# Kernel optimization log

Measured on AMD Instinct MI355X. Metric: run time of the kernel, lower is better.

Reference implementation:

```python
import jax, jax.numpy as jnp
import numpy as np

B, N, DIM, H, DH, P = 4, 4096, 256, 8, 64, 2
INNER = H * DH  # 512


def setup_inputs() -> dict:
    key = jax.random.key(0)
    ks = jax.random.split(key, 10)
    w = lambda k, shape: jax.random.normal(k, shape, dtype=jnp.float32) * 0.02
    return dict(
        x=jax.random.normal(ks[0], (B, N, DIM), dtype=jnp.float32),
        prev_x=jax.random.normal(ks[1], (B, N, DIM), dtype=jnp.float32),
        ln_q_g=jnp.ones((2 * DIM,), jnp.float32), ln_q_b=jnp.zeros((2 * DIM,), jnp.float32),
        ln_k_g=jnp.ones((DIM,), jnp.float32), ln_k_b=jnp.zeros((DIM,), jnp.float32),
        ln_v_g=jnp.ones((DIM,), jnp.float32), ln_v_b=jnp.zeros((DIM,), jnp.float32),
        Wq=w(ks[2], (2 * DIM, INNER)),            # to_q, bias=False
        Wk=w(ks[3], (DIM, INNER)), bk=jnp.zeros((INNER,), jnp.float32),
        Wv=w(ks[4], (DIM, INNER)), bv=jnp.zeros((INNER,), jnp.float32),
        Woff=w(ks[5], (H * P, INNER)),            # 1x1 conv == linear over channels
        boff=jax.random.uniform(ks[6], (H * P,), jnp.float32, -1.0, 1.0),
        Wout=w(ks[7], (DIM, INNER)), bout=jnp.zeros((DIM,), jnp.float32),
    )


def _ln(x, g, b):
    m = x.mean(-1, keepdims=True)
    v = ((x - m) ** 2).mean(-1, keepdims=True)
    return (x - m) * jax.lax.rsqrt(v + 1e-5) * g + b


def reference(x, prev_x, ln_q_g, ln_q_b, ln_k_g, ln_k_b, ln_v_g, ln_v_b,
              Wq, Wk, bk, Wv, bv, Woff, boff, Wout, bout):
    scale = DH ** -0.5
    # queries from cat(x, prev_x) along feature dim
    q = _ln(jnp.concatenate([x, prev_x], axis=-1), ln_q_g, ln_q_b) @ Wq  # (B,N,INNER)
    # learned per-head, per-point offsets (1x1 conv over channels)
    offsets = (q @ Woff.T + boff).reshape(B, N, H, P).transpose(0, 2, 3, 1)  # (B,H,P,N)
    # K/V from cat(x, prev_x) along batch dim -> KV length 2N per (b,h)
    kv = jnp.concatenate([x, prev_x], axis=0)  # (2B,N,DIM)
    k = (_ln(kv, ln_k_g, ln_k_b) @ Wk + bk).reshape(2, B, N, H, DH).transpose(1, 3, 4, 0, 2).reshape(B, H, DH, 2 * N)
    v = (_ln(kv, ln_v_g, ln_v_b) @ Wv + bv).reshape(2, B, N, H, DH).transpose(1, 3, 4, 0, 2).reshape(B, H, DH, 2 * N)
    # sampling positions: pos + offset, clamped, truncated to int (matches torch .long())
    pos = jnp.arange(N, dtype=jnp.float32)
    samp = jnp.clip(pos[None, None, None, :] + offsets, 0, 2 * N - 1).astype(jnp.int32)  # (B,H,P,N)
    idx = samp.transpose(0, 1, 3, 2)[:, :, None, :, :]  # (B,H,1,N,P)
    k_s = jnp.take_along_axis(k[:, :, :, None, :], idx, axis=-1)  # (B,H,DH,N,P)
    v_s = jnp.take_along_axis(v[:, :, :, None, :], idx, axis=-1)  # (B,H,DH,N,P)
    qh = q.reshape(B, N, H, DH).transpose(0, 2, 1, 3) * scale     # (B,H,N,DH)
    sim = jnp.einsum('bhnd,bhdnp->bhnp', qh, k_s)                  # (B,H,N,P)
    attn = jax.nn.softmax(sim, axis=-1)
    out = jnp.einsum('bhnp,bhdnp->bhnd', attn, v_s)                # (B,H,N,DH)
    out = out.transpose(0, 2, 1, 3).reshape(B, N, INNER) @ Wout.T + bout  # (B,N,DIM)
    return out, offsets
```

## Files before the change

### kernel.cpp

```cpp
#include <hip/hip_runtime.h>
#include <hip/hip_bf16.h>
#include <math.h>

#define B_    4
#define N_    4096
#define DIM_  256
#define H_    8
#define DH_   64
#define P_    2
#define INNER_ 512
#define BN_   (B_ * N_)
#define KVR_  (2 * BN_)
#define VOFF_ ((size_t)H_ * KVR_ * DH_)

typedef short v8s  __attribute__((ext_vector_type(8)));
typedef short v4s  __attribute__((ext_vector_type(4)));
typedef float v4f  __attribute__((ext_vector_type(4)));

__device__ __forceinline__ short f2b(float x) {
    __hip_bfloat16 h = __float2bfloat16(x);
    return *reinterpret_cast<short*>(&h);
}
__device__ __forceinline__ float b2f(short s) {
    __hip_bfloat16 h = *reinterpret_cast<__hip_bfloat16*>(&s);
    return __bfloat162float(h);
}

__device__ __forceinline__ void async16(const void* g, void* l) {
    __builtin_amdgcn_global_load_lds(
        (const __attribute__((address_space(1))) void*)g,
        (__attribute__((address_space(3))) void*)l, 16, 0, 0);
}

__device__ __forceinline__ void storeRow(float* p, float4 f0, float4 f1, float4 f2, float4 f3) {
    ((float4*)p)[0] = f0; ((float4*)p)[1] = f1; ((float4*)p)[2] = f2; ((float4*)p)[3] = f3;
}
__device__ __forceinline__ void storeRowS(short* p, float4 f0, float4 f1, float4 f2, float4 f3) {
    v8s o0, o1;
    o0[0]=f2b(f0.x); o0[1]=f2b(f0.y); o0[2]=f2b(f0.z); o0[3]=f2b(f0.w);
    o0[4]=f2b(f1.x); o0[5]=f2b(f1.y); o0[6]=f2b(f1.z); o0[7]=f2b(f1.w);
    o1[0]=f2b(f2.x); o1[1]=f2b(f2.y); o1[2]=f2b(f2.z); o1[3]=f2b(f2.w);
    o1[4]=f2b(f3.x); o1[5]=f2b(f3.y); o1[6]=f2b(f3.z); o1[7]=f2b(f3.w);
    ((v8s*)p)[0] = o0; ((v8s*)p)[1] = o1;
}

__global__ __launch_bounds__(256) void prep_all(
    const float* __restrict__ Wq, const float* __restrict__ gq, const float* __restrict__ betaq,
    const float* __restrict__ Wk, const float* __restrict__ gk, const float* __restrict__ betak,
    const float* __restrict__ bk,
    const float* __restrict__ Wv, const float* __restrict__ gv, const float* __restrict__ betav,
    const float* __restrict__ bv,
    const float* __restrict__ Woff, const float* __restrict__ Wout,
    short* __restrict__ Wq2t, float* __restrict__ bq2,
    short* __restrict__ Wkvt, float* __restrict__ bkv,
    float* __restrict__ Wcomb, float* __restrict__ braw, short* __restrict__ Woutb) {
    __shared__ float sm[272];
    const int bid = blockIdx.x, t = threadIdx.x;

    if (bid < 1536) {
        const float *W, *g, *beta, *bias_in;
        short* Wt; float* b2; int K, n; float scale;
        if (bid < 512)       { W=Wq; g=gq; beta=betaq; bias_in=nullptr; Wt=Wq2t; b2=bq2; K=512; n=bid;        scale=0.125f; }
        else if (bid < 1024) { W=Wk; g=gk; beta=betak; bias_in=bk; Wt=Wkvt;           b2=bkv;       K=256; n=bid-512;  scale=1.f; }
        else                 { W=Wv; g=gv; beta=betav; bias_in=bv; Wt=Wkvt+512*256;   b2=bkv+512;   K=256; n=bid-1024; scale=1.f; }
        float partial = 0.f;
        for (int k = t; k < K; k += 256) {
            float w = W[k * 512 + n];
            Wt[(size_t)n * K + k] = f2b(scale * g[k] * w);
            partial += beta[k] * w;
        }
        sm[t] = partial;
        __syncthreads();
        for (int s = 128; s > 0; s >>= 1) {
            if (t < s) sm[t] += sm[t + s];
            __syncthreads();
        }
        if (t == 0) b2[n] = scale * ((bias_in ? bias_in[n] : 0.f) + sm[0]);
    } else if (bid < 2048) {
        const int k = bid - 1536;
        const int hp = t & 15, jg = t >> 4;
        float p = 0.f;
        for (int j = jg; j < INNER_; j += 16)
            p += Wq[k * INNER_ + j] * Woff[hp * INNER_ + j];
        sm[jg * 17 + hp] = p;
        __syncthreads();
        if (t < 16) {
            float s = 0.f;
            for (int i = 0; i < 16; i++) s += sm[i * 17 + t];
            Wcomb[k * 16 + t] = gq[k] * s;
            braw[k * 16 + t]  = betaq[k] * s;
        }
    } else {
        const int i0 = (bid - 2048) * 1024 + t * 4;
        float4 f = *(const float4*)(Wout + i0);
        v4s o;
        o[0] = f2b(f.x); o[1] = f2b(f.y); o[2] = f2b(f.z); o[3] = f2b(f.w);
        *(v4s*)(Woutb + i0) = o;
    }
}

__global__ __launch_bounds__(256) void norm_fused_kernel(
    const float* __restrict__ x, const float* __restrict__ p,
    const float* __restrict__ Wcomb, const float* __restrict__ braw,
    const float* __restrict__ boff,
    short* __restrict__ Aq, short* __restrict__ Akv,
    float* __restrict__ out_off, int* __restrict__ idx) {
    __shared__ float smr[272];
    __shared__ float sc[4][4][16][33];
    const int t    = threadIdx.x;
    const int lane = t & 63;
    const int wv   = t >> 6;
    const int m0   = (blockIdx.x * 4 + wv) * 4;
    const int k8   = lane * 8;

    {
        const int hp = t & 15, kg = t >> 4;
        float pp = 0.f;
        for (int k = kg; k < 512; k += 16) pp += braw[k * 16 + hp];
        smr[kg * 17 + hp] = pp;
    }
    __syncthreads();
    if (t < 16) {
        float s = 0.f;
#pragma unroll
        for (int i = 0; i < 16; i++) s += smr[i * 17 + t];
        smr[256 + t] = s + boff[t];
    }
    __syncthreads();

    float4 w[8][4];
#pragma unroll
    for (int i = 0; i < 8; i++) {
        const float4* wr = (const float4*)(Wcomb + (size_t)(k8 + i) * 16);
#pragma unroll
        for (int j = 0; j < 4; j++) w[i][j] = wr[j];
    }

    const float* srcb = (lane < 32) ? (x + k8) : (p + k8 - DIM_);

    float4 ua[4][2];
#pragma unroll
    for (int r = 0; r < 4; r++) {
        ua[r][0] = ((const float4*)(srcb + (size_t)(m0 + r) * DIM_))[0];
        ua[r][1] = ((const float4*)(srcb + (size_t)(m0 + r) * DIM_))[1];
    }

    float s[4], q2[4];
#pragma unroll
    for (int r = 0; r < 4; r++) {
        float uv[8] = { ua[r][0].x, ua[r][0].y, ua[r][0].z, ua[r][0].w,
                        ua[r][1].x, ua[r][1].y, ua[r][1].z, ua[r][1].w };
        float ss = 0.f, qq = 0.f;
#pragma unroll
        for (int i = 0; i < 8; i++) { ss += uv[i]; qq += uv[i] * uv[i]; }
        s[r] = ss; q2[r] = qq;
    }
#pragma unroll
    for (int d = 1; d <= 16; d <<= 1) {
#pragma unroll
        for (int r = 0; r < 4; r++) {
            s[r]  += __shfl_xor(s[r], d);
            q2[r] += __shfl_xor(q2[r], d);
        }
    }
    float mean_h[4], rstd_h[4], mean_q[4], rstd_q[4];
#pragma unroll
    for (int r = 0; r < 4; r++) {
        mean_h[r] = s[r] * (1.f / 256.f);
        float var_h = q2[r] * (1.f / 256.f) - mean_h[r] * mean_h[r];
        rstd_h[r] = rsqrtf(var_h + 1e-5f);
        float sf  = s[r]  + __shfl_xor(s[r], 32);
        float q2f = q2[r] + __shfl_xor(q2[r], 32);
        mean_q[r] = sf * (1.f / 512.f);
        float var_q = q2f * (1.f / 512.f) - mean_q[r] * mean_q[r];
        rstd_q[r] = rsqrtf(var_q + 1e-5f);
    }

#pragma unroll
    for (int r = 0; r < 4; r++) {
        const int m = m0 + r;
        float uv[8] = { ua[r][0].x, ua[r][0].y, ua[r][0].z, ua[r][0].w,
                        ua[r][1].x, ua[r][1].y, ua[r][1].z, ua[r][1].w };

        v8s okv;
#pragma unroll
        for (int i = 0; i < 8; i++) okv[i] = f2b((uv[i] - mean_h[r]) * rstd_h[r]);
        short* akvdst = Akv + ((lane < 32) ? ((size_t)m * DIM_ + k8)
                                           : ((size_t)(BN_ + m) * DIM_ + k8 - DIM_));
        *(v8s*)akvdst = okv;

        float nv[8];
        v8s oq;
#pragma unroll
        for (int i = 0; i < 8; i++) { nv[i] = (uv[i] - mean_q[r]) * rstd_q[r]; oq[i] = f2b(nv[i]); }
        *(v8s*)(Aq + (size_t)m * INNER_ + k8) = oq;

        float acc[16];
#pragma unroll
        for (int h = 0; h < 16; h++) acc[h] = 0.f;
#pragma unroll
        for (int i = 0; i < 8; i++) {
            float nvi = nv[i];
            acc[0]  += nvi * w[i][0].x;  acc[1]  += nvi * w[i][0].y;
            acc[2]  += nvi * w[i][0].z;  acc[3]  += nvi * w[i][0].w;
            acc[4]  += nvi * w[i][1].x;  acc[5]  += nvi * w[i][1].y;
            acc[6]  += nvi * w[i][1].z;  acc[7]  += nvi * w[i][1].w;
            acc[8]  += nvi * w[i][2].x;  acc[9]  += nvi * w[i][2].y;
            acc[10] += nvi * w[i][2].z;  acc[11] += nvi * w[i][2].w;
            acc[12] += nvi * w[i][3].x;  acc[13] += nvi * w[i][3].y;
            acc[14] += nvi * w[i][3].z;  acc[15] += nvi * w[i][3].w;
        }
#pragma unroll
        for (int j = 0; j < 16; j++) acc[j] += __shfl_xor(acc[j], 32);
        if (lane < 32) {
#pragma unroll
            for (int j = 0; j < 16; j++) sc[wv][r][j][lane] = acc[j];
        }
    }
    asm volatile("s_waitcnt lgkmcnt(0)" ::: "memory");

    {
        const int r3 = lane >> 4, j3 = lane & 15;
        const float* sp = &sc[wv][r3][j3][0];
        float4 p0 = *(const float4*)(sp + 0),  p1 = *(const float4*)(sp + 4);
        float4 p2 = *(const float4*)(sp + 8),  p3 = *(const float4*)(sp + 12);
        float4 p4 = *(const float4*)(sp + 16), p5 = *(const float4*)(sp + 20);
        float4 p6 = *(const float4*)(sp + 24), p7 = *(const float4*)(sp + 28);
        float sx = ((p0.x + p1.x) + (p2.x + p3.x)) + ((p4.x + p5.x) + (p6.x + p7.x));
        float sy = ((p0.y + p1.y) + (p2.y + p3.y)) + ((p4.y + p5.y) + (p6.y + p7.y));
        float sz = ((p0.z + p1.z) + (p2.z + p3.z)) + ((p4.z + p5.z) + (p6.z + p7.z));
        float sw = ((p0.w + p1.w) + (p2.w + p3.w)) + ((p4.w + p5.w) + (p6.w + p7.w));
        float off = (sx + sy) + (sz + sw) + smr[256 + j3];

        const int m = m0 + r3;
        const int b = m >> 12, n = m & (N_ - 1);
        const int h = j3 >> 1, pp = j3 & 1;
        out_off[(size_t)((b * H_ + h) * P_ + pp) * N_ + n] = off;
        float f = fminf(fmaxf((float)n + off, 0.f), (float)(2 * N_ - 1));
        idx[((size_t)(b * H_ + h) * N_ + n) * P_ + pp] = (int)f;
    }
}

template <typename OT>
__device__ __forceinline__ void gemm_body(
    short* smem, const short* __restrict__ A, const short* __restrict__ Bt,
    const float* __restrict__ bias, OT* __restrict__ C, int N, int K, int nx, int lin) {
    short* As = smem;
    short* Bs = smem + 128 * 64;
    const int tid  = threadIdx.x;
    const int lane = tid & 63, w = tid >> 6;
    const int wr = w >> 1, wc = w & 1;
    const int lm = lane & 15, g = lane >> 4;

    const int x8 = lin & 7, t = lin >> 3;
    const int bx = t % nx, by = (t / nx) * 8 + x8;
    const int row0 = by * 128, col0 = bx * 128;

    const short* pa[4];
    const short* pb[4];
#pragma unroll
    for (int r = 0; r < 4; r++) {
        int s   = tid + 256 * r;
        int row = s >> 3, kcs = s & 7;
        int kg  = kcs ^ (row & 7);
        pa[r] = A  + (size_t)(row0 + row) * K + kg * 8;
        pb[r] = Bt + (size_t)(col0 + row) * K + kg * 8;
    }

    v4f acc[4][4];
#pragma unroll
    for (int i = 0; i < 4; i++)
#pragma unroll
        for (int j = 0; j < 4; j++) acc[i][j] = (v4f){0.f, 0.f, 0.f, 0.f};

    for (int k0 = 0; k0 < K; k0 += 64) {
        __syncthreads();
#pragma unroll
        for (int r = 0; r < 4; r++) {
            int s = tid + 256 * r;
            async16(pa[r] + k0, (char*)As + s * 16);
            async16(pb[r] + k0, (char*)Bs + s * 16);
        }
        __syncthreads();
#pragma unroll
        for (int ks = 0; ks < 2; ks++) {
            v8s af[4], bf[4];
#pragma unroll
            for (int i = 0; i < 4; i++) {
                int m   = wr * 64 + i * 16 + lm;
                int sch = m * 8 + ((ks * 4 + g) ^ (m & 7));
                af[i] = *(const v8s*)(As + sch * 8);
            }
#pragma unroll
            for (int j = 0; j < 4; j++) {
                int n   = wc * 64 + j * 16 + lm;
                int sch = n * 8 + ((ks * 4 + g) ^ (n & 7));
                bf[j] = *(const v8s*)(Bs + sch * 8);
            }
#pragma unroll
            for (int i = 0; i < 4; i++)
#pragma unroll
                for (int j = 0; j < 4; j++)
                    acc[i][j] = __builtin_amdgcn_mfma_f32_16x16x32_bf16(af[i], bf[j], acc[i][j], 0, 0, 0);
        }
    }

#pragma unroll
    for (int j = 0; j < 4; j++) {
        int gc = col0 + wc * 64 + j * 16 + lm;
        float bj = bias ? bias[gc] : 0.f;
#pragma unroll
        for (int i = 0; i < 4; i++)
#pragma unroll
            for (int r = 0; r < 4; r++) acc[i][j][r] += bj;
    }

    __syncthreads();
    float* ep = (float*)smem + w * (16 * 68);
#pragma unroll
    for (int i = 0; i < 4; i++) {
#pragma unroll
        for (int j = 0; j < 4; j++)
#pragma unroll
            for (int r = 0; r < 4; r++)
                ep[(g * 4 + r) * 68 + j * 16 + lm] = acc[i][j][r];
        asm volatile("s_waitcnt lgkmcnt(0)" ::: "memory");
        int rr = lane >> 2, cb = (lane & 3) * 16;
        float4 f0 = *(float4*)(ep + rr * 68 + cb + 0);
        float4 f1 = *(float4*)(ep + rr * 68 + cb + 4);
        float4 f2 = *(float4*)(ep + rr * 68 + cb + 8);
        float4 f3 = *(float4*)(ep + rr * 68 + cb + 12);
        asm volatile("s_waitcnt lgkmcnt(0)" ::: "memory");
        int grow = row0 + wr * 64 + i * 16 + rr;
        int gcol = col0 + wc * 64 + cb;
        storeRow(&C[(size_t)grow * N + gcol], f0, f1, f2, f3);
    }
}

#define ATILE_ (256 * 64)

__global__ __launch_bounds__(512, 2) void gemm_qkv_256(
    const short* __restrict__ Aqp, const short* __restrict__ Wq2t,
    const float* __restrict__ bq2, short* __restrict__ qbh,
    const short* __restrict__ Akvp, const short* __restrict__ Wkvt,
    const float* __restrict__ bkv, short* __restrict__ khv) {
    __shared__ short smem[4 * ATILE_];

    const short* A; const short* Bt; const float* bias; short* C;
    int K, NT, nxs, nwg, lin;
    bool isQ;
    if ((int)blockIdx.x < 128) {
        A = Aqp;  Bt = Wq2t; bias = bq2; C = qbh;
        K = 512; NT = 8; nxs = 1; nwg = 128; lin = blockIdx.x; isQ = true;
    } else {
        A = Akvp; Bt = Wkvt; bias = bkv; C = khv;
        K = 256; NT = 4; nxs = 2; nwg = 512; lin = blockIdx.x - 128; isQ = false;
    }

    const int tid  = threadIdx.x;
    const int lane = tid & 63, w = tid >> 6;
    const int wr = w >> 2, wc = w & 3;
    const int lm = lane & 15, g = lane >> 4;

    const int wg = (lin & 7) * (nwg >> 3) + (lin >> 3);
    const int bx = wg & ((1 << nxs) - 1), by = wg >> nxs;
    const int row0 = by << 8, col0 = bx << 8;

    short* As0 = smem;
    short* Bs0 = smem + 2 * ATILE_;

    const int kg = ((tid & 7) ^ ((tid >> 3) & 7)) << 3;
    const short* gA = A  + (size_t)(row0 + (tid >> 3)) * K + kg;
    const short* gB = Bt + (size_t)(col0 + (tid >> 3)) * K + kg;

    auto stageA = [&](int buf, int k0) {
        char* lp = (char*)(As0 + buf * ATILE_);
#pragma unroll
        for (int r = 0; r < 4; r++)
            async16(gA + (size_t)r * 64 * K + k0, lp + r * 8192 + tid * 16);
    };
    auto stageB = [&](int buf, int k0) {
        char* lp = (char*)(Bs0 + buf * ATILE_);
#pragma unroll
        for (int r = 0; r < 4; r++)
            async16(gB + (size_t)r * 64 * K + k0, lp + r * 8192 + tid * 16);
    };

    v4f acc[8][4];
#pragma unroll
    for (int i = 0; i < 8; i++)
#pragma unroll
        for (int j = 0; j < 4; j++) acc[i][j] = (v4f){0.f, 0.f, 0.f, 0.f};

    float bj[4];
#pragma unroll
    for (int jj = 0; jj < 4; jj++) bj[jj] = bias[col0 + wc * 64 + jj * 16 + lm];

    v8s aLo[4][2], aHi[4][2], bF[4][2];

    auto RD_A = [&](const short* base, int half, v8s (*dst)[2]) {
#pragma unroll
        for (int i = 0; i < 4; i++) {
            const int m = wr * 128 + half * 64 + i * 16 + lm;
#pragma unroll
            for (int ks = 0; ks < 2; ks++)
                dst[i][ks] = *(const v8s*)(base + m * 64 + (((ks << 2) | g) ^ (m & 7)) * 8);
        }
    };
    auto RD_B = [&](const short* base) {
#pragma unroll
        for (int j = 0; j < 4; j++) {
            const int n = wc * 64 + j * 16 + lm;
#pragma unroll
            for (int ks = 0; ks < 2; ks++)
                bF[j][ks] = *(const v8s*)(base + n * 64 + (((ks << 2) | g) ^ (n & 7)) * 8);
        }
    };
    auto MFMA_H = [&](int half, v8s (*af)[2]) {
        __builtin_amdgcn_s_setprio(1);
#pragma unroll
        for (int i = 0; i < 4; i++)
#pragma unroll
            for (int j = 0; j < 4; j++) {
                acc[half*4+i][j] = __builtin_amdgcn_mfma_f32_16x16x32_bf16(af[i][0], bF[j][0], acc[half*4+i][j], 0, 0, 0);
                acc[half*4+i][j] = __builtin_amdgcn_mfma_f32_16x16x32_bf16(af[i][1], bF[j][1], acc[half*4+i][j], 0, 0, 0);
            }
        __builtin_amdgcn_s_setprio(0);
    };

    stageB(0, 0); stageA(0, 0);
    stageB(1, 64); stageA(1, 64);
    asm volatile("s_waitcnt vmcnt(8)" ::: "memory");
    __builtin_amdgcn_s_barrier();
    asm volatile("" ::: "memory");

    for (int T = 0; T < NT; ++T) {
        const int cur = T & 1;
        const short* as = As0 + cur * ATILE_;
        const short* bs = Bs0 + cur * ATILE_;
        const bool s2 = (T + 2 < NT);
        const int k2 = (T + 2) << 6;

        RD_B(bs);
        RD_A(as, 0, aLo);
        asm volatile("s_waitcnt lgkmcnt(0)" ::: "memory");
        __builtin_amdgcn_s_barrier();
        if (s2) stageB(cur, k2);
        MFMA_H(0, aLo);
        RD_A(as, 1, aHi);
        asm volatile("s_waitcnt lgkmcnt(0)" ::: "memory");
        __builtin_amdgcn_s_barrier();
        if (s2) stageA(cur, k2);
        MFMA_H(1, aHi);
        if (s2)              asm volatile("s_waitcnt vmcnt(8)" ::: "memory");
        else if (T + 1 < NT) asm volatile("s_waitcnt vmcnt(0)" ::: "memory");
        __builtin_amdgcn_s_barrier();
        asm volatile("" ::: "memory");
    }

    float* ep = (float*)smem + w * (16 * 68);
#pragma unroll
    for (int ii = 0; ii < 8; ii++) {
#pragma unroll
        for (int jj = 0; jj < 4; jj++)
#pragma unroll
            for (int r = 0; r < 4; r++)
                ep[(g * 4 + r) * 68 + jj * 16 + lm] = acc[ii][jj][r] + bj[jj];
        asm volatile("s_waitcnt lgkmcnt(0)" ::: "memory");
        const int rr = lane >> 2, cb = (lane & 3) * 16;
        float4 f0 = *(float4*)(ep + rr * 68 + cb + 0);
        float4 f1 = *(float4*)(ep + rr * 68 + cb + 4);
        float4 f2 = *(float4*)(ep + rr * 68 + cb + 8);
        float4 f3 = *(float4*)(ep + rr * 68 + cb + 12);
        asm volatile("s_waitcnt lgkmcnt(0)" ::: "memory");
        const int grow = row0 + wr * 128 + ii * 16 + rr;
        const int gcol = col0 + wc * 64 + cb;
        short* dst;
        if (isQ) {
            const int h = gcol >> 6;
            dst = C + ((size_t)h * BN_ + grow) * DH_ + (gcol & 63);
        } else {
            const size_t base = (gcol < 512) ? 0 : VOFF_;
            const int h = (gcol >> 6) & 7;
            dst = C + base + ((size_t)h * KVR_ + grow) * DH_ + (gcol & 63);
        }
        storeRowS(dst, f0, f1, f2, f3);
    }
}

__global__ __launch_bounds__(256) void gemm_out(
    const short* __restrict__ A, const short* __restrict__ Bt,
    const float* __restrict__ bias, float* __restrict__ C) {
    __shared__ short smem[2 * 128 * 64];
    const int lin = blockIdx.y * gridDim.x + blockIdx.x;
    gemm_body<float>(smem, A, Bt, bias, C, 256, 512, 2, lin);
}

__global__ __launch_bounds__(256) void attn_kernel(
    const short* __restrict__ qbh, const short* __restrict__ khv,
    const int* __restrict__ idx, short* __restrict__ attnout) {
    const int lane = threadIdx.x & 63;
    const int wv   = threadIdx.x >> 6;
    const int s    = lane >> 4, c = lane & 15;
    const int n = blockIdx.x * 16 + wv * 4 + s;
    const int h = blockIdx.y, b = blockIdx.z;
    const int m = b * N_ + n;

    v4s qv = *(const v4s*)(qbh + ((size_t)h * BN_ + m) * DH_ + c * 4);

    const int* ip = idx + ((size_t)(b * H_ + h) * N_ + n) * P_;
    int j0 = ip[0], j1 = ip[1];
    int r0 = b * N_ + j0 + ((j0 >= N_) ? (BN_ - N_) : 0);
    int r1 = b * N_ + j1 + ((j1 >= N_) ? (BN_ - N_) : 0);
    const short* k0p = khv + ((size_t)h * KVR_ + r0) * DH_ + c * 4;
    const short* k1p = khv + ((size_t)h * KVR_ + r1) * DH_ + c * 4;
    v4s k0 = *(const v4s*)k0p, v0 = *(const v4s*)(k0p + VOFF_);
    v4s k1 = *(const v4s*)k1p, v1 = *(const v4s*)(k1p + VOFF_);

    float q0 = b2f(qv[0]), q1 = b2f(qv[1]), q2 = b2f(qv[2]), q3 = b2f(qv[3]);
    float s0 = q0 * b2f(k0[0]) + q1 * b2f(k0[1]) + q2 * b2f(k0[2]) + q3 * b2f(k0[3]);
    float s1 = q0 * b2f(k1[0]) + q1 * b2f(k1[1]) + q2 * b2f(k1[2]) + q3 * b2f(k1[3]);
#pragma unroll
    for (int d = 1; d <= 8; d <<= 1) {
        s0 += __shfl_xor(s0, d);
        s1 += __shfl_xor(s1, d);
    }
    float mx = fmaxf(s0, s1);
    float e0 = __expf(s0 - mx), e1 = __expf(s1 - mx);
    float inv = 1.f / (e0 + e1);
    v4s o;
#pragma unroll
    for (int i = 0; i < 4; i++)
        o[i] = f2b((e0 * b2f(v0[i]) + e1 * b2f(v1[i])) * inv);
    *(v4s*)(attnout + (size_t)m * INNER_ + h * DH_ + c * 4) = o;
}

extern "C" void kernel_launch(void* const* d_in, const int* in_sizes, int n_in,
                              void* d_out, int out_size, void* d_ws, size_t ws_size,
                              hipStream_t stream) {
    (void)in_sizes; (void)n_in; (void)out_size; (void)ws_size;

    const float* x      = (const float*)d_in[0];
    const float* prevx  = (const float*)d_in[1];
    const float* ln_q_g = (const float*)d_in[2];
    const float* ln_q_b = (const float*)d_in[3];
    const float* ln_k_g = (const float*)d_in[4];
    const float* ln_k_b = (const float*)d_in[5];
    const float* ln_v_g = (const float*)d_in[6];
    const float* ln_v_b = (const float*)d_in[7];
    const float* Wq     = (const float*)d_in[8];
    const float* Wk     = (const float*)d_in[9];
    const float* bk     = (const float*)d_in[10];
    const float* Wv     = (const float*)d_in[11];
    const float* bv     = (const float*)d_in[12];
    const float* Woff   = (const float*)d_in[13];
    const float* boff   = (const float*)d_in[14];
    const float* Wout   = (const float*)d_in[15];
    const float* bout   = (const float*)d_in[16];

    char* cur = (char*)d_ws;
    auto alloc = [&](size_t bytes) { char* p = cur; cur += (bytes + 255) & ~(size_t)255; return p; };
    short* Aq      = (short*)alloc((size_t)BN_ * INNER_ * 2);
    short* Akv     = (short*)alloc((size_t)KVR_ * DIM_ * 2);
    short* qbh     = (short*)alloc((size_t)BN_ * INNER_ * 2);
    short* khv     = (short*)alloc((size_t)KVR_ * 1024 * 2);
    short* attnout = (short*)alloc((size_t)BN_ * INNER_ * 2);
    short* Wq2t    = (short*)alloc(512 * 512 * 2);
    short* Wkvt    = (short*)alloc(1024 * 256 * 2);
    short* Woutb   = (short*)alloc(256 * 512 * 2);
    float* bq2     = (float*)alloc(512 * 4);
    float* bkv     = (float*)alloc(1024 * 4);
    float* Wcomb   = (float*)alloc(512 * 16 * 4);
    float* braw    = (float*)alloc(512 * 16 * 4);
    int*   idxb    = (int*)alloc((size_t)BN_ * 16 * 4);

    float* out_main = (float*)d_out;
    float* out_off  = out_main + (size_t)BN_ * DIM_;

    prep_all<<<2176, 256, 0, stream>>>(Wq, ln_q_g, ln_q_b,
                                       Wk, ln_k_g, ln_k_b, bk,
                                       Wv, ln_v_g, ln_v_b, bv,
                                       Woff, Wout,
                                       Wq2t, bq2, Wkvt, bkv, Wcomb, braw, Woutb);

    norm_fused_kernel<<<BN_ / 16, 256, 0, stream>>>(x, prevx, Wcomb, braw, boff,
                                                    Aq, Akv, out_off, idxb);

    gemm_qkv_256<<<640, 512, 0, stream>>>(Aq, Wq2t, bq2, qbh,
                                          Akv, Wkvt, bkv, khv);

    dim3 ga(N_ / 16, H_, B_);
    attn_kernel<<<ga, 256, 0, stream>>>(qbh, khv, idxb, attnout);

    gemm_out<<<dim3(2, 128), 256, 0, stream>>>(attnout, Woutb, bout, out_main);
}
```

Baseline: 219.5 us.

## Pre-tile weights into MFMA fragment layout and load B straight from global

The prep kernel now writes the transposed Q/K/V weights in a per-16-column, per-64-K tile fragment order. The QKV GEMM then loads B fragments directly from global memory into registers instead of staging them through LDS. This halves the GEMM's shared memory and removes the B staging and LDS reads. The price is global and L2 latency inside the K loop, and the explicit vmcnt waits that guarded the async A staging are gone. A separate change moves a __syncthreads in the offset kernel later, so the bias reduction overlaps the weight loads.

```diff
diff --git a/kernel.cpp b/kernel.cpp
--- a/kernel.cpp
+++ b/kernel.cpp
@@ -59,14 +59,17 @@
 
     if (bid < 1536) {
         const float *W, *g, *beta, *bias_in;
-        short* Wt; float* b2; int K, n; float scale;
-        if (bid < 512)       { W=Wq; g=gq; beta=betaq; bias_in=nullptr; Wt=Wq2t; b2=bq2; K=512; n=bid;        scale=0.125f; }
-        else if (bid < 1024) { W=Wk; g=gk; beta=betak; bias_in=bk; Wt=Wkvt;           b2=bkv;       K=256; n=bid-512;  scale=1.f; }
-        else                 { W=Wv; g=gv; beta=betav; bias_in=bv; Wt=Wkvt+512*256;   b2=bkv+512;   K=256; n=bid-1024; scale=1.f; }
+        short* Wt; float* b2; int K, n, ng; float scale;
+        if (bid < 512)       { W=Wq; g=gq; beta=betaq; bias_in=nullptr; Wt=Wq2t; b2=bq2; K=512; n=bid;       ng=n;          scale=0.125f; }
+        else if (bid < 1024) { W=Wk; g=gk; beta=betak; bias_in=bk; Wt=Wkvt; b2=bkv;       K=256; n=bid-512;  ng=n;          scale=1.f; }
+        else                 { W=Wv; g=gv; beta=betav; bias_in=bv; Wt=Wkvt; b2=bkv+512;   K=256; n=bid-1024; ng=n+512;      scale=1.f; }
+        const int NT = K >> 6;
+        const int jt = ng >> 4, lmn = ng & 15;
         float partial = 0.f;
         for (int k = t; k < K; k += 256) {
             float w = W[k * 512 + n];
-            Wt[(size_t)n * K + k] = f2b(scale * g[k] * w);
+            const int T = k >> 6, chunk = (k >> 3) & 7, e = k & 7;
+            Wt[(size_t)(((jt * NT + T) * 8 + chunk) * 128 + lmn * 8 + e)] = f2b(scale * g[k] * w);
             partial += beta[k] * w;
         }
         sm[t] = partial;
@@ -126,7 +129,6 @@
         for (int i = 0; i < 16; i++) s += smr[i * 17 + t];
         smr[256 + t] = s + boff[t];
     }
-    __syncthreads();
 
     float4 w[8][4];
 #pragma unroll
@@ -218,6 +220,7 @@
         }
     }
     asm volatile("s_waitcnt lgkmcnt(0)" ::: "memory");
+    __syncthreads();
 
     {
         const int r3 = lane >> 4, j3 = lane & 15;
@@ -344,7 +347,7 @@
     const float* __restrict__ bq2, short* __restrict__ qbh,
     const short* __restrict__ Akvp, const short* __restrict__ Wkvt,
     const float* __restrict__ bkv, short* __restrict__ khv) {
-    __shared__ short smem[4 * ATILE_];
+    __shared__ short smem[2 * ATILE_];
 
     const short* A; const short* Bt; const float* bias; short* C;
     int K, NT, nxs, nwg, lin;
@@ -367,11 +370,9 @@
     const int row0 = by << 8, col0 = bx << 8;
 
     short* As0 = smem;
-    short* Bs0 = smem + 2 * ATILE_;
 
     const int kg = ((tid & 7) ^ ((tid >> 3) & 7)) << 3;
-    const short* gA = A  + (size_t)(row0 + (tid >> 3)) * K + kg;
-    const short* gB = Bt + (size_t)(col0 + (tid >> 3)) * K + kg;
+    const short* gA = A + (size_t)(row0 + (tid >> 3)) * K + kg;
 
     auto stageA = [&](int buf, int k0) {
         char* lp = (char*)(As0 + buf * ATILE_);
@@ -379,12 +380,9 @@
         for (int r = 0; r < 4; r++)
             async16(gA + (size_t)r * 64 * K + k0, lp + r * 8192 + tid * 16);
     };
-    auto stageB = [&](int buf, int k0) {
-        char* lp = (char*)(Bs0 + buf * ATILE_);
-#pragma unroll
-        for (int r = 0; r < 4; r++)
-            async16(gB + (size_t)r * 64 * K + k0, lp + r * 8192 + tid * 16);
-    };
+
+    const v8s* Bp = (const v8s*)Bt;
+    const int jt0 = bx * 16 + wc * 4;
 
     v4f acc[8][4];
 #pragma unroll
@@ -405,15 +403,6 @@
 #pragma unroll
             for (int ks = 0; ks < 2; ks++)
                 dst[i][ks] = *(const v8s*)(base + m * 64 + (((ks << 2) | g) ^ (m & 7)) * 8);
-        }
-    };
-    auto RD_B = [&](const short* base) {
-#pragma unroll
-        for (int j = 0; j < 4; j++) {
-            const int n = wc * 64 + j * 16 + lm;
-#pragma unroll
-            for (int ks = 0; ks < 2; ks++)
-                bF[j][ks] = *(const v8s*)(base + n * 64 + (((ks << 2) | g) ^ (n & 7)) * 8);
         }
     };
     auto MFMA_H = [&](int half, v8s (*af)[2]) {
@@ -428,32 +417,29 @@
         __builtin_amdgcn_s_setprio(0);
     };
 
-    stageB(0, 0); stageA(0, 0);
-    stageB(1, 64); stageA(1, 64);
-    asm volatile("s_waitcnt vmcnt(8)" ::: "memory");
+    stageA(0, 0);
+    stageA(1, 64);
+    asm volatile("s_waitcnt vmcnt(4)" ::: "memory");
     __builtin_amdgcn_s_barrier();
     asm volatile("" ::: "memory");
 
     for (int T = 0; T < NT; ++T) {
         const int cur = T & 1;
         const short* as = As0 + cur * ATILE_;
-        const short* bs = Bs0 + cur * ATILE_;
-        const bool s2 = (T + 2 < NT);
-        const int k2 = (T + 2) << 6;
-
-        RD_B(bs);
+
+#pragma unroll
+        for (int j = 0; j < 4; j++)
+#pragma unroll
+            for (int ks = 0; ks < 2; ks++)
+                bF[j][ks] = Bp[(size_t)(jt0 + j) * NT * 128 + (size_t)T * 128 + ((ks << 2) | g) * 16 + lm];
+
         RD_A(as, 0, aLo);
-        asm volatile("s_waitcnt lgkmcnt(0)" ::: "memory");
-        __builtin_amdgcn_s_barrier();
-        if (s2) stageB(cur, k2);
-        MFMA_H(0, aLo);
         RD_A(as, 1, aHi);
         asm volatile("s_waitcnt lgkmcnt(0)" ::: "memory");
         __builtin_amdgcn_s_barrier();
-        if (s2) stageA(cur, k2);
+        if (T + 2 < NT) stageA(cur, (T + 2) << 6);
+        MFMA_H(0, aLo);
         MFMA_H(1, aHi);
-        if (s2)              asm volatile("s_waitcnt vmcnt(8)" ::: "memory");
-        else if (T + 1 < NT) asm volatile("s_waitcnt vmcnt(0)" ::: "memory");
         __builtin_amdgcn_s_barrier();
         asm volatile("" ::: "memory");
     }
```

New measurement: 236.5 us. 7.8% more time.

## Fuse deformable attention gather with output projection GEMM in one kernel

Applied to the files above, without the earlier changes.

The separate attention kernel and output GEMM are merged. Each block now computes the attention output for 64 rows across all heads into a swizzled LDS tile, then multiplies it by Wout with double-buffered async loads of the weight tiles. This removes the global round-trip of the attention output and one kernel launch. In exchange the grid shrinks to 256 blocks using a large LDS footprint, which limits occupancy. A barrier in the norm kernel is also moved later so the weight loads can overlap the bias reduction.

```diff
diff --git a/kernel.cpp b/kernel.cpp
--- a/kernel.cpp
+++ b/kernel.cpp
@@ -126,7 +126,6 @@
         for (int i = 0; i < 16; i++) s += smr[i * 17 + t];
         smr[256 + t] = s + boff[t];
     }
-    __syncthreads();
 
     float4 w[8][4];
 #pragma unroll
@@ -218,6 +217,7 @@
         }
     }
     asm volatile("s_waitcnt lgkmcnt(0)" ::: "memory");
+    __syncthreads();
 
     {
         const int r3 = lane >> 4, j3 = lane & 15;
@@ -241,102 +241,6 @@
     }
 }
 
-template <typename OT>
-__device__ __forceinline__ void gemm_body(
-    short* smem, const short* __restrict__ A, const short* __restrict__ Bt,
-    const float* __restrict__ bias, OT* __restrict__ C, int N, int K, int nx, int lin) {
-    short* As = smem;
-    short* Bs = smem + 128 * 64;
-    const int tid  = threadIdx.x;
-    const int lane = tid & 63, w = tid >> 6;
-    const int wr = w >> 1, wc = w & 1;
-    const int lm = lane & 15, g = lane >> 4;
-
-    const int x8 = lin & 7, t = lin >> 3;
-    const int bx = t % nx, by = (t / nx) * 8 + x8;
-    const int row0 = by * 128, col0 = bx * 128;
-
-    const short* pa[4];
-    const short* pb[4];
-#pragma unroll
-    for (int r = 0; r < 4; r++) {
-        int s   = tid + 256 * r;
-        int row = s >> 3, kcs = s & 7;
-        int kg  = kcs ^ (row & 7);
-        pa[r] = A  + (size_t)(row0 + row) * K + kg * 8;
-        pb[r] = Bt + (size_t)(col0 + row) * K + kg * 8;
-    }
-
-    v4f acc[4][4];
-#pragma unroll
-    for (int i = 0; i < 4; i++)
-#pragma unroll
-        for (int j = 0; j < 4; j++) acc[i][j] = (v4f){0.f, 0.f, 0.f, 0.f};
-
-    for (int k0 = 0; k0 < K; k0 += 64) {
-        __syncthreads();
-#pragma unroll
-        for (int r = 0; r < 4; r++) {
-            int s = tid + 256 * r;
-            async16(pa[r] + k0, (char*)As + s * 16);
-            async16(pb[r] + k0, (char*)Bs + s * 16);
-        }
-        __syncthreads();
-#pragma unroll
-        for (int ks = 0; ks < 2; ks++) {
-            v8s af[4], bf[4];
-#pragma unroll
-            for (int i = 0; i < 4; i++) {
-                int m   = wr * 64 + i * 16 + lm;
-                int sch = m * 8 + ((ks * 4 + g) ^ (m & 7));
-                af[i] = *(const v8s*)(As + sch * 8);
-            }
-#pragma unroll
-            for (int j = 0; j < 4; j++) {
-                int n   = wc * 64 + j * 16 + lm;
-                int sch = n * 8 + ((ks * 4 + g) ^ (n & 7));
-                bf[j] = *(const v8s*)(Bs + sch * 8);
-            }
-#pragma unroll
-            for (int i = 0; i < 4; i++)
-#pragma unroll
-                for (int j = 0; j < 4; j++)
-                    acc[i][j] = __builtin_amdgcn_mfma_f32_16x16x32_bf16(af[i], bf[j], acc[i][j], 0, 0, 0);
-        }
-    }
-
-#pragma unroll
-    for (int j = 0; j < 4; j++) {
-        int gc = col0 + wc * 64 + j * 16 + lm;
-        float bj = bias ? bias[gc] : 0.f;
-#pragma unroll
-        for (int i = 0; i < 4; i++)
-#pragma unroll
-            for (int r = 0; r < 4; r++) acc[i][j][r] += bj;
-    }
-
-    __syncthreads();
-    float* ep = (float*)smem + w * (16 * 68);
-#pragma unroll
-    for (int i = 0; i < 4; i++) {
-#pragma unroll
-        for (int j = 0; j < 4; j++)
-#pragma unroll
-            for (int r = 0; r < 4; r++)
-                ep[(g * 4 + r) * 68 + j * 16 + lm] = acc[i][j][r];
-        asm volatile("s_waitcnt lgkmcnt(0)" ::: "memory");
-        int rr = lane >> 2, cb = (lane & 3) * 16;
-        float4 f0 = *(float4*)(ep + rr * 68 + cb + 0);
-        float4 f1 = *(float4*)(ep + rr * 68 + cb + 4);
-        float4 f2 = *(float4*)(ep + rr * 68 + cb + 8);
-        float4 f3 = *(float4*)(ep + rr * 68 + cb + 12);
-        asm volatile("s_waitcnt lgkmcnt(0)" ::: "memory");
-        int grow = row0 + wr * 64 + i * 16 + rr;
-        int gcol = col0 + wc * 64 + cb;
-        storeRow(&C[(size_t)grow * N + gcol], f0, f1, f2, f3);
-    }
-}
-
 #define ATILE_ (256 * 64)
 
 __global__ __launch_bounds__(512, 2) void gemm_qkv_256(
@@ -488,51 +392,139 @@
     }
 }
 
-__global__ __launch_bounds__(256) void gemm_out(
-    const short* __restrict__ A, const short* __restrict__ Bt,
-    const float* __restrict__ bias, float* __restrict__ C) {
-    __shared__ short smem[2 * 128 * 64];
-    const int lin = blockIdx.y * gridDim.x + blockIdx.x;
-    gemm_body<float>(smem, A, Bt, bias, C, 256, 512, 2, lin);
-}
-
-__global__ __launch_bounds__(256) void attn_kernel(
+__global__ __launch_bounds__(256) void attn_out_kernel(
     const short* __restrict__ qbh, const short* __restrict__ khv,
-    const int* __restrict__ idx, short* __restrict__ attnout) {
-    const int lane = threadIdx.x & 63;
-    const int wv   = threadIdx.x >> 6;
-    const int s    = lane >> 4, c = lane & 15;
-    const int n = blockIdx.x * 16 + wv * 4 + s;
-    const int h = blockIdx.y, b = blockIdx.z;
-    const int m = b * N_ + n;
-
-    v4s qv = *(const v4s*)(qbh + ((size_t)h * BN_ + m) * DH_ + c * 4);
-
-    const int* ip = idx + ((size_t)(b * H_ + h) * N_ + n) * P_;
-    int j0 = ip[0], j1 = ip[1];
-    int r0 = b * N_ + j0 + ((j0 >= N_) ? (BN_ - N_) : 0);
-    int r1 = b * N_ + j1 + ((j1 >= N_) ? (BN_ - N_) : 0);
-    const short* k0p = khv + ((size_t)h * KVR_ + r0) * DH_ + c * 4;
-    const short* k1p = khv + ((size_t)h * KVR_ + r1) * DH_ + c * 4;
-    v4s k0 = *(const v4s*)k0p, v0 = *(const v4s*)(k0p + VOFF_);
-    v4s k1 = *(const v4s*)k1p, v1 = *(const v4s*)(k1p + VOFF_);
-
-    float q0 = b2f(qv[0]), q1 = b2f(qv[1]), q2 = b2f(qv[2]), q3 = b2f(qv[3]);
-    float s0 = q0 * b2f(k0[0]) + q1 * b2f(k0[1]) + q2 * b2f(k0[2]) + q3 * b2f(k0[3]);
-    float s1 = q0 * b2f(k1[0]) + q1 * b2f(k1[1]) + q2 * b2f(k1[2]) + q3 * b2f(k1[3]);
-#pragma unroll
-    for (int d = 1; d <= 8; d <<= 1) {
-        s0 += __shfl_xor(s0, d);
-        s1 += __shfl_xor(s1, d);
-    }
-    float mx = fmaxf(s0, s1);
-    float e0 = __expf(s0 - mx), e1 = __expf(s1 - mx);
-    float inv = 1.f / (e0 + e1);
-    v4s o;
+    const int* __restrict__ idx, const short* __restrict__ Woutb,
+    const float* __restrict__ bout, float* __restrict__ C) {
+    __shared__ short As[64 * 512];
+    __shared__ short Bs[2][256 * 64];
+    const int tid  = threadIdx.x;
+    const int lane = tid & 63, wv = tid >> 6;
+    const int sg   = lane >> 4, c = lane & 15;
+    const int lm   = c, g = sg;
+    const int m0   = blockIdx.x * 64;
+
+#pragma unroll 2
+    for (int pass = 0; pass < 32; ++pass) {
+        const int task = pass * 16 + wv * 4 + sg;
+        const int mloc = task >> 3, h = task & 7;
+        const int m = m0 + mloc;
+        const int b = m >> 12, n = m & (N_ - 1);
+
+        v4s qv = *(const v4s*)(qbh + ((size_t)h * BN_ + m) * DH_ + c * 4);
+        const int* ip = idx + ((size_t)(b * H_ + h) * N_ + n) * P_;
+        int j0 = ip[0], j1 = ip[1];
+        int r0 = b * N_ + j0 + ((j0 >= N_) ? (BN_ - N_) : 0);
+        int r1 = b * N_ + j1 + ((j1 >= N_) ? (BN_ - N_) : 0);
+        const short* k0p = khv + ((size_t)h * KVR_ + r0) * DH_ + c * 4;
+        const short* k1p = khv + ((size_t)h * KVR_ + r1) * DH_ + c * 4;
+        v4s k0 = *(const v4s*)k0p, v0 = *(const v4s*)(k0p + VOFF_);
+        v4s k1 = *(const v4s*)k1p, v1 = *(const v4s*)(k1p + VOFF_);
+
+        float q0 = b2f(qv[0]), q1 = b2f(qv[1]), q2 = b2f(qv[2]), q3 = b2f(qv[3]);
+        float s0 = q0 * b2f(k0[0]) + q1 * b2f(k0[1]) + q2 * b2f(k0[2]) + q3 * b2f(k0[3]);
+        float s1 = q0 * b2f(k1[0]) + q1 * b2f(k1[1]) + q2 * b2f(k1[2]) + q3 * b2f(k1[3]);
+#pragma unroll
+        for (int d = 1; d <= 8; d <<= 1) {
+            s0 += __shfl_xor(s0, d);
+            s1 += __shfl_xor(s1, d);
+        }
+        float mx = fmaxf(s0, s1);
+        float e0 = __expf(s0 - mx), e1 = __expf(s1 - mx);
+        float inv = 1.f / (e0 + e1);
+        v4s o;
+#pragma unroll
+        for (int i = 0; i < 4; i++)
+            o[i] = f2b((e0 * b2f(v0[i]) + e1 * b2f(v1[i])) * inv);
+        const int g0  = h * 8 + (c >> 1);
+        const int swz = g0 ^ (mloc & 7);
+        *(v4s*)(As + mloc * 512 + swz * 8 + (c & 1) * 4) = o;
+    }
+    __syncthreads();
+
+    auto stageB = [&](int buf, int T) {
+#pragma unroll
+        for (int r = 0; r < 8; r++) {
+            int sI = tid + 256 * r;
+            int row = sI >> 3, kc = sI & 7;
+            int kgg = kc ^ (row & 7);
+            async16(Woutb + (size_t)row * 512 + T * 64 + kgg * 8,
+                    (char*)(&Bs[buf][0]) + sI * 16);
+        }
+    };
+
+    v4f acc[4][4];
 #pragma unroll
     for (int i = 0; i < 4; i++)
-        o[i] = f2b((e0 * b2f(v0[i]) + e1 * b2f(v1[i])) * inv);
-    *(v4s*)(attnout + (size_t)m * INNER_ + h * DH_ + c * 4) = o;
+#pragma unroll
+        for (int j = 0; j < 4; j++) acc[i][j] = (v4f){0.f, 0.f, 0.f, 0.f};
+
+    float bj[4];
+#pragma unroll
+    for (int j = 0; j < 4; j++) bj[j] = bout[wv * 64 + j * 16 + lm];
+
+    stageB(0, 0); stageB(1, 1);
+    asm volatile("s_waitcnt vmcnt(8)" ::: "memory");
+    __builtin_amdgcn_s_barrier();
+    asm volatile("" ::: "memory");
+
+    for (int T = 0; T < 8; ++T) {
+        const int cur = T & 1;
+        v8s af[4][2], bf[4][2];
+#pragma unroll
+        for (int i = 0; i < 4; i++) {
+            const int m = i * 16 + lm;
+#pragma unroll
+            for (int ks = 0; ks < 2; ks++) {
+                const int gr = T * 8 + (((ks << 2) | g) ^ (m & 7));
+                af[i][ks] = *(const v8s*)(As + m * 512 + gr * 8);
+            }
+        }
+#pragma unroll
+        for (int j = 0; j < 4; j++) {
+            const int col = wv * 64 + j * 16 + lm;
+#pragma unroll
+            for (int ks = 0; ks < 2; ks++)
+                bf[j][ks] = *(const v8s*)(&Bs[cur][0] + col * 64 + ((((ks << 2) | g)) ^ (col & 7)) * 8);
+        }
+        asm volatile("s_waitcnt lgkmcnt(0)" ::: "memory");
+        __builtin_amdgcn_s_barrier();
+        if (T + 2 < 8) stageB(cur, T + 2);
+        __builtin_amdgcn_s_setprio(1);
+#pragma unroll
+        for (int i = 0; i < 4; i++)
+#pragma unroll
+            for (int j = 0; j < 4; j++) {
+                acc[i][j] = __builtin_amdgcn_mfma_f32_16x16x32_bf16(af[i][0], bf[j][0], acc[i][j], 0, 0, 0);
+                acc[i][j] = __builtin_amdgcn_mfma_f32_16x16x32_bf16(af[i][1], bf[j][1], acc[i][j], 0, 0, 0);
+            }
+        __builtin_amdgcn_s_setprio(0);
+        if (T + 2 < 8)      asm volatile("s_waitcnt vmcnt(8)" ::: "memory");
+        else if (T + 1 < 8) asm volatile("s_waitcnt vmcnt(0)" ::: "memory");
+        __builtin_amdgcn_s_barrier();
+        asm volatile("" ::: "memory");
+    }
+
+    __syncthreads();
+    float* ep = (float*)As + wv * (16 * 68);
+#pragma unroll
+    for (int i = 0; i < 4; i++) {
+#pragma unroll
+        for (int j = 0; j < 4; j++)
+#pragma unroll
+            for (int r = 0; r < 4; r++)
+                ep[(g * 4 + r) * 68 + j * 16 + lm] = acc[i][j][r] + bj[j];
+        asm volatile("s_waitcnt lgkmcnt(0)" ::: "memory");
+        const int rr = lane >> 2, cb = (lane & 3) * 16;
+        float4 f0 = *(float4*)(ep + rr * 68 + cb + 0);
+        float4 f1 = *(float4*)(ep + rr * 68 + cb + 4);
+        float4 f2 = *(float4*)(ep + rr * 68 + cb + 8);
+        float4 f3 = *(float4*)(ep + rr * 68 + cb + 12);
+        asm volatile("s_waitcnt lgkmcnt(0)" ::: "memory");
+        const int grow = m0 + i * 16 + rr;
+        const int gcol = wv * 64 + cb;
+        storeRow(&C[(size_t)grow * DIM_ + gcol], f0, f1, f2, f3);
+    }
 }
 
 extern "C" void kernel_launch(void* const* d_in, const int* in_sizes, int n_in,
@@ -564,7 +556,6 @@
     short* Akv     = (short*)alloc((size_t)KVR_ * DIM_ * 2);
     short* qbh     = (short*)alloc((size_t)BN_ * INNER_ * 2);
     short* khv     = (short*)alloc((size_t)KVR_ * 1024 * 2);
-    short* attnout = (short*)alloc((size_t)BN_ * INNER_ * 2);
     short* Wq2t    = (short*)alloc(512 * 512 * 2);
     short* Wkvt    = (short*)alloc(1024 * 256 * 2);
     short* Woutb   = (short*)alloc(256 * 512 * 2);
@@ -589,8 +580,5 @@
     gemm_qkv_256<<<640, 512, 0, stream>>>(Aq, Wq2t, bq2, qbh,
                                           Akv, Wkvt, bkv, khv);
 
-    dim3 ga(N_ / 16, H_, B_);
-    attn_kernel<<<ga, 256, 0, stream>>>(qbh, khv, idxb, attnout);
-
-    gemm_out<<<dim3(2, 128), 256, 0, stream>>>(attnout, Woutb, bout, out_main);
-}
+    attn_out_kernel<<<256, 256, 0, stream>>>(qbh, khv, idxb, Woutb, bout, out_main);
+}
```

Result: slower. 227.9 us (+3.8%).

## Store QKV projections row-major and hoist offset-bias reduction into its own kernel

Applied to the files above, without the earlier changes.

The QKV GEMM now writes Q as a plain (BN, 512) row-major matrix and K/V interleaved as (2BN, 1024) rows, instead of head-major scattered layouts. The attention kernel indexes these row-major buffers, so K and V for a sampled row sit in the same 2KB row. A separate single-block kernel precomputes the combined offset bias, so each norm block no longer repeats that reduction and two barriers. The cost is one extra launch and less contiguous per-head gathers in attention.

```diff
diff --git a/kernel.cpp b/kernel.cpp
--- a/kernel.cpp
+++ b/kernel.cpp
@@ -11,7 +11,6 @@
 #define INNER_ 512
 #define BN_   (B_ * N_)
 #define KVR_  (2 * BN_)
-#define VOFF_ ((size_t)H_ * KVR_ * DH_)
 
 typedef short v8s  __attribute__((ext_vector_type(8)));
 typedef short v4s  __attribute__((ext_vector_type(4)));
@@ -35,7 +34,7 @@
 __device__ __forceinline__ void storeRow(float* p, float4 f0, float4 f1, float4 f2, float4 f3) {
     ((float4*)p)[0] = f0; ((float4*)p)[1] = f1; ((float4*)p)[2] = f2; ((float4*)p)[3] = f3;
 }
-__device__ __forceinline__ void storeRowS(short* p, float4 f0, float4 f1, float4 f2, float4 f3) {
+__device__ __forceinline__ void storeRow(__hip_bfloat16* p, float4 f0, float4 f1, float4 f2, float4 f3) {
     v8s o0, o1;
     o0[0]=f2b(f0.x); o0[1]=f2b(f0.y); o0[2]=f2b(f0.z); o0[3]=f2b(f0.w);
     o0[4]=f2b(f1.x); o0[5]=f2b(f1.y); o0[6]=f2b(f1.z); o0[7]=f2b(f1.w);
@@ -99,34 +98,33 @@
     }
 }
 
+__global__ void bcomb_sum(const float* __restrict__ braw, const float* __restrict__ boff,
+                          float* __restrict__ bcomb) {
+    __shared__ float sm[272];
+    int t = threadIdx.x;
+    int hp = t & 15, kg = t >> 4;
+    float p = 0.f;
+    for (int k = kg; k < 512; k += 16) p += braw[k * 16 + hp];
+    sm[kg * 17 + hp] = p;
+    __syncthreads();
+    if (t < 16) {
+        float s = 0.f;
+        for (int i = 0; i < 16; i++) s += sm[i * 17 + t];
+        bcomb[t] = s + boff[t];
+    }
+}
+
 __global__ __launch_bounds__(256) void norm_fused_kernel(
     const float* __restrict__ x, const float* __restrict__ p,
-    const float* __restrict__ Wcomb, const float* __restrict__ braw,
-    const float* __restrict__ boff,
+    const float* __restrict__ Wcomb, const float* __restrict__ bcomb,
     short* __restrict__ Aq, short* __restrict__ Akv,
     float* __restrict__ out_off, int* __restrict__ idx) {
-    __shared__ float smr[272];
     __shared__ float sc[4][4][16][33];
     const int t    = threadIdx.x;
     const int lane = t & 63;
     const int wv   = t >> 6;
     const int m0   = (blockIdx.x * 4 + wv) * 4;
     const int k8   = lane * 8;
-
-    {
-        const int hp = t & 15, kg = t >> 4;
-        float pp = 0.f;
-        for (int k = kg; k < 512; k += 16) pp += braw[k * 16 + hp];
-        smr[kg * 17 + hp] = pp;
-    }
-    __syncthreads();
-    if (t < 16) {
-        float s = 0.f;
-#pragma unroll
-        for (int i = 0; i < 16; i++) s += smr[i * 17 + t];
-        smr[256 + t] = s + boff[t];
-    }
-    __syncthreads();
 
     float4 w[8][4];
 #pragma unroll
@@ -230,7 +228,7 @@
         float sy = ((p0.y + p1.y) + (p2.y + p3.y)) + ((p4.y + p5.y) + (p6.y + p7.y));
         float sz = ((p0.z + p1.z) + (p2.z + p3.z)) + ((p4.z + p5.z) + (p6.z + p7.z));
         float sw = ((p0.w + p1.w) + (p2.w + p3.w)) + ((p4.w + p5.w) + (p6.w + p7.w));
-        float off = (sx + sy) + (sz + sw) + smr[256 + j3];
+        float off = (sx + sy) + (sz + sw) + bcomb[j3];
 
         const int m = m0 + r3;
         const int b = m >> 12, n = m & (N_ - 1);
@@ -341,20 +339,19 @@
 
 __global__ __launch_bounds__(512, 2) void gemm_qkv_256(
     const short* __restrict__ Aqp, const short* __restrict__ Wq2t,
-    const float* __restrict__ bq2, short* __restrict__ qbh,
+    const float* __restrict__ bq2, __hip_bfloat16* __restrict__ qb,
     const short* __restrict__ Akvp, const short* __restrict__ Wkvt,
-    const float* __restrict__ bkv, short* __restrict__ khv) {
+    const float* __restrict__ bkv, __hip_bfloat16* __restrict__ kvproj) {
     __shared__ short smem[4 * ATILE_];
 
-    const short* A; const short* Bt; const float* bias; short* C;
-    int K, NT, nxs, nwg, lin;
-    bool isQ;
+    const short* A; const short* Bt; const float* bias; __hip_bfloat16* C;
+    int N, K, NT, nxs, nwg, lin;
     if ((int)blockIdx.x < 128) {
-        A = Aqp;  Bt = Wq2t; bias = bq2; C = qbh;
-        K = 512; NT = 8; nxs = 1; nwg = 128; lin = blockIdx.x; isQ = true;
+        A = Aqp;  Bt = Wq2t; bias = bq2; C = qb;
+        N = 512;  K = 512; NT = 8; nxs = 1; nwg = 128; lin = blockIdx.x;
     } else {
-        A = Akvp; Bt = Wkvt; bias = bkv; C = khv;
-        K = 256; NT = 4; nxs = 2; nwg = 512; lin = blockIdx.x - 128; isQ = false;
+        A = Akvp; Bt = Wkvt; bias = bkv; C = kvproj;
+        N = 1024; K = 256; NT = 4; nxs = 2; nwg = 512; lin = blockIdx.x - 128;
     }
 
     const int tid  = threadIdx.x;
@@ -475,16 +472,7 @@
         asm volatile("s_waitcnt lgkmcnt(0)" ::: "memory");
         const int grow = row0 + wr * 128 + ii * 16 + rr;
         const int gcol = col0 + wc * 64 + cb;
-        short* dst;
-        if (isQ) {
-            const int h = gcol >> 6;
-            dst = C + ((size_t)h * BN_ + grow) * DH_ + (gcol & 63);
-        } else {
-            const size_t base = (gcol < 512) ? 0 : VOFF_;
-            const int h = (gcol >> 6) & 7;
-            dst = C + base + ((size_t)h * KVR_ + grow) * DH_ + (gcol & 63);
-        }
-        storeRowS(dst, f0, f1, f2, f3);
+        storeRow(&C[(size_t)grow * N + gcol], f0, f1, f2, f3);
     }
 }
 
@@ -497,7 +485,7 @@
 }
 
 __global__ __launch_bounds__(256) void attn_kernel(
-    const short* __restrict__ qbh, const short* __restrict__ khv,
+    const short* __restrict__ qb, const short* __restrict__ kvproj,
     const int* __restrict__ idx, short* __restrict__ attnout) {
     const int lane = threadIdx.x & 63;
     const int wv   = threadIdx.x >> 6;
@@ -506,16 +494,16 @@
     const int h = blockIdx.y, b = blockIdx.z;
     const int m = b * N_ + n;
 
-    v4s qv = *(const v4s*)(qbh + ((size_t)h * BN_ + m) * DH_ + c * 4);
+    v4s qv = *(const v4s*)(qb + (size_t)m * INNER_ + h * DH_ + c * 4);
 
     const int* ip = idx + ((size_t)(b * H_ + h) * N_ + n) * P_;
     int j0 = ip[0], j1 = ip[1];
     int r0 = b * N_ + j0 + ((j0 >= N_) ? (BN_ - N_) : 0);
     int r1 = b * N_ + j1 + ((j1 >= N_) ? (BN_ - N_) : 0);
-    const short* k0p = khv + ((size_t)h * KVR_ + r0) * DH_ + c * 4;
-    const short* k1p = khv + ((size_t)h * KVR_ + r1) * DH_ + c * 4;
-    v4s k0 = *(const v4s*)k0p, v0 = *(const v4s*)(k0p + VOFF_);
-    v4s k1 = *(const v4s*)k1p, v1 = *(const v4s*)(k1p + VOFF_);
+    const short* k0p = kvproj + (size_t)r0 * 1024 + h * DH_ + c * 4;
+    const short* k1p = kvproj + (size_t)r1 * 1024 + h * DH_ + c * 4;
+    v4s k0 = *(const v4s*)k0p, v0 = *(const v4s*)(k0p + 512);
+    v4s k1 = *(const v4s*)k1p, v1 = *(const v4s*)(k1p + 512);
 
     float q0 = b2f(qv[0]), q1 = b2f(qv[1]), q2 = b2f(qv[2]), q3 = b2f(qv[3]);
     float s0 = q0 * b2f(k0[0]) + q1 * b2f(k0[1]) + q2 * b2f(k0[2]) + q3 * b2f(k0[3]);
@@ -562,8 +550,8 @@
     auto alloc = [&](size_t bytes) { char* p = cur; cur += (bytes + 255) & ~(size_t)255; return p; };
     short* Aq      = (short*)alloc((size_t)BN_ * INNER_ * 2);
     short* Akv     = (short*)alloc((size_t)KVR_ * DIM_ * 2);
-    short* qbh     = (short*)alloc((size_t)BN_ * INNER_ * 2);
-    short* khv     = (short*)alloc((size_t)KVR_ * 1024 * 2);
+    short* qb      = (short*)alloc((size_t)BN_ * INNER_ * 2);
+    short* kvproj  = (short*)alloc((size_t)KVR_ * 1024 * 2);
     short* attnout = (short*)alloc((size_t)BN_ * INNER_ * 2);
     short* Wq2t    = (short*)alloc(512 * 512 * 2);
     short* Wkvt    = (short*)alloc(1024 * 256 * 2);
@@ -572,6 +560,7 @@
     float* bkv     = (float*)alloc(1024 * 4);
     float* Wcomb   = (float*)alloc(512 * 16 * 4);
     float* braw    = (float*)alloc(512 * 16 * 4);
+    float* bcomb   = (float*)alloc(16 * 4);
     int*   idxb    = (int*)alloc((size_t)BN_ * 16 * 4);
 
     float* out_main = (float*)d_out;
@@ -582,15 +571,16 @@
                                        Wv, ln_v_g, ln_v_b, bv,
                                        Woff, Wout,
                                        Wq2t, bq2, Wkvt, bkv, Wcomb, braw, Woutb);
-
-    norm_fused_kernel<<<BN_ / 16, 256, 0, stream>>>(x, prevx, Wcomb, braw, boff,
+    bcomb_sum<<<1, 256, 0, stream>>>(braw, boff, bcomb);
+
+    norm_fused_kernel<<<BN_ / 16, 256, 0, stream>>>(x, prevx, Wcomb, bcomb,
                                                     Aq, Akv, out_off, idxb);
 
-    gemm_qkv_256<<<640, 512, 0, stream>>>(Aq, Wq2t, bq2, qbh,
-                                          Akv, Wkvt, bkv, khv);
+    gemm_qkv_256<<<640, 512, 0, stream>>>(Aq, Wq2t, bq2, (__hip_bfloat16*)qb,
+                                          Akv, Wkvt, bkv, (__hip_bfloat16*)kvproj);
 
     dim3 ga(N_ / 16, H_, B_);
-    attn_kernel<<<ga, 256, 0, stream>>>(qbh, khv, idxb, attnout);
+    attn_kernel<<<ga, 256, 0, stream>>>(qb, kvproj, idxb, attnout);
 
     gemm_out<<<dim3(2, 128), 256, 0, stream>>>(attnout, Woutb, bout, out_main);
 }
```

New measurement: 214.7 us. 2.1% less time.
